# Kernel optimization log

Hardware: AMD Instinct MI355X
Metric: run time of the kernel (lower is better)

The kernel has to match this reference:

```python
import jax, jax.numpy as jnp
import numpy as np

LOG2 = float(np.log(2.0))

def ssp(x):
    # ShiftedSoftplus: softplus(x) - log(2)
    return jax.nn.softplus(x) - LOG2

B, N, F, R, P = 8, 1000, 128, 20, 512000  # batch, atoms, n_atom_basis=n_filters, n_rbf, n_pairs

def setup_inputs() -> dict:
    key = jax.random.key(0)
    ks = jax.random.split(key, 14)
    inv = lambda d: 1.0 / np.sqrt(d)
    return {
        "x": jax.random.normal(ks[0], (B, N, F), dtype=jnp.float32),
        "f_ij": jax.random.normal(ks[1], (P, R), dtype=jnp.float32),
        "idx_i": jax.random.randint(ks[2], (P,), 0, B * N, dtype=jnp.int32),
        "idx_j": jax.random.randint(ks[3], (P,), 0, B * N, dtype=jnp.int32),
        "rcut_ij": jax.random.uniform(ks[4], (P,), dtype=jnp.float32),
        # input_to_feature: Linear(F, F)
        "W_in": jax.random.normal(ks[5], (F, F), dtype=jnp.float32) * inv(F),
        "b_in": jnp.zeros((F,), dtype=jnp.float32),
        # filter_network: Linear(R, F) -> SSP -> Linear(F, F)
        "Wf1": jax.random.normal(ks[6], (R, F), dtype=jnp.float32) * inv(R),
        "bf1": jnp.zeros((F,), dtype=jnp.float32),
        "Wf2": jax.random.normal(ks[7], (F, F), dtype=jnp.float32) * inv(F),
        "bf2": jnp.zeros((F,), dtype=jnp.float32),
        # feature_to_output: Linear(F, F) -> SSP -> Linear(F, F)
        "Wo1": jax.random.normal(ks[8], (F, F), dtype=jnp.float32) * inv(F),
        "bo1": jnp.zeros((F,), dtype=jnp.float32),
        "Wo2": jax.random.normal(ks[9], (F, F), dtype=jnp.float32) * inv(F),
        "bo2": jnp.zeros((F,), dtype=jnp.float32),
    }

def reference(x, f_ij, idx_i, idx_j, rcut_ij,
              W_in, b_in, Wf1, bf1, Wf2, bf2, Wo1, bo1, Wo2, bo2):
    batch, n_atoms = x.shape[0], x.shape[1]
    # input_to_feature
    h = (x @ W_in + b_in).reshape(batch * n_atoms, -1)      # [B*N, F]
    # filter network on radial basis, modulated by cutoff
    Wij = ssp(f_ij @ Wf1 + bf1) @ Wf2 + bf2                 # [P, F]
    Wij = Wij * rcut_ij[:, None]
    # gather neighbor features, elementwise filter, scatter-add to center atom
    x_ij = h[idx_j] * Wij                                   # [P, F]
    agg = jax.ops.segment_sum(x_ij, idx_i, num_segments=batch * n_atoms)  # [B*N, F]
    # feature_to_output
    out = ssp(agg @ Wo1 + bo1) @ Wo2 + bo2
    return out.reshape(batch, n_atoms, 128)
```

## Files before the change

### kernel.cpp

```cpp
#include <hip/hip_runtime.h>
#include <hip/hip_bf16.h>
#include <math.h>

#define FDIM 128
#define RDIM 20
#define BN   8000
#define NPAIR 512000
#define PB   64
#define ROWS 8

typedef __attribute__((ext_vector_type(8))) short short8v;
typedef __attribute__((ext_vector_type(4))) float float4v;

__device__ __forceinline__ float sspf_fast(float x) {
    return fmaxf(x, 0.0f) + __logf(1.0f + __expf(-fabsf(x))) - 0.69314718055994531f;
}
__device__ __forceinline__ float sspf(float x) {
    return fmaxf(x, 0.0f) + log1pf(expf(-fabsf(x))) - 0.69314718055994531f;
}

__device__ __forceinline__ unsigned short bfs(float a) {
    union { __hip_bfloat16 h; unsigned short u; } v;
    v.h = __float2bfloat16(a);
    return v.u;
}
__device__ __forceinline__ unsigned pkbf(float a, float b) {
    union { __hip_bfloat162 h; unsigned u; } v;
    v.h = __float22bfloat162_rn(make_float2(a, b));
    return v.u;
}

__global__ __launch_bounds__(256) void hist_kernel(
    const int* __restrict__ idx_i, int* __restrict__ cnt)
{
    const int p = blockIdx.x * 256 + threadIdx.x;
    if (p < NPAIR) atomicAdd(&cnt[idx_i[p]], 1);
}

__global__ __launch_bounds__(1024) void scan_kernel(
    const int* __restrict__ cnt, int* __restrict__ cursor)
{
    __shared__ int part[1024];
    const int t = threadIdx.x;
    int v[8]; int sum = 0;
    #pragma unroll
    for (int k = 0; k < 8; ++k) {
        const int i = t * 8 + k;
        const int c = (i < BN) ? cnt[i] : 0;
        v[k] = sum; sum += c;
    }
    part[t] = sum;
    __syncthreads();
    for (int off = 1; off < 1024; off <<= 1) {
        const int x = (t >= off) ? part[t - off] : 0;
        __syncthreads();
        part[t] += x;
        __syncthreads();
    }
    const int base = (t == 0) ? 0 : part[t - 1];
    #pragma unroll
    for (int k = 0; k < 8; ++k) {
        const int i = t * 8 + k;
        if (i < BN) cursor[i] = base + v[k];
    }
}

__global__ __launch_bounds__(256) void scatter_kernel(
    const int* __restrict__ idx_i, int* __restrict__ cursor, int* __restrict__ perm)
{
    const int p = blockIdx.x * 256 + threadIdx.x;
    if (p < NPAIR) {
        const int pos = atomicAdd(&cursor[idx_i[p]], 1);
        perm[pos] = p;
    }
}

__global__ __launch_bounds__(256) void scatter_split(
    const int* __restrict__ idx_i, const int* __restrict__ idx_j,
    int* __restrict__ cursor, int4* __restrict__ msorted)
{
    const int p = blockIdx.x * 256 + threadIdx.x;
    if (p < NPAIR) {
        const int ii = idx_i[p];
        const int pos = atomicAdd(&cursor[ii], 1);
        msorted[pos] = make_int4(p, idx_j[p], ii & (ROWS - 1), 0);
    }
}

template<bool SSP, bool BF16OUT>
__global__ __launch_bounds__(256) void rowgemm_kernel(
    const float* __restrict__ A, const float* __restrict__ W,
    const float* __restrict__ bias, void* __restrict__ Cv)
{
    __shared__ float rowlds[16 * 128];
    const int tid = threadIdx.x;
    const int blk = blockIdx.x;
    for (int s = tid; s < 16 * 128; s += 256)
        rowlds[s] = A[blk * 16 * 128 + s];
    __syncthreads();

    const int lane = tid & 63;
    const int wave = tid >> 6;
    const float b0 = bias[lane];
    const float b1 = bias[64 + lane];
    float acc[4][2];
    #pragma unroll
    for (int rr = 0; rr < 4; ++rr) { acc[rr][0] = b0; acc[rr][1] = b1; }

    #pragma unroll 4
    for (int m = 0; m < 128; ++m) {
        const float w0 = W[m * 128 + lane];
        const float w1 = W[m * 128 + 64 + lane];
        #pragma unroll
        for (int rr = 0; rr < 4; ++rr) {
            const float av = rowlds[(wave * 4 + rr) * 128 + m];
            acc[rr][0] = fmaf(av, w0, acc[rr][0]);
            acc[rr][1] = fmaf(av, w1, acc[rr][1]);
        }
    }

    #pragma unroll
    for (int rr = 0; rr < 4; ++rr) {
        const int p = blk * 16 + wave * 4 + rr;
        float v0 = acc[rr][0], v1 = acc[rr][1];
        if (SSP) { v0 = sspf(v0); v1 = sspf(v1); }
        if (BF16OUT) {
            unsigned short* C = (unsigned short*)Cv;
            C[p * 128 + lane]      = bfs(v0);
            C[p * 128 + 64 + lane] = bfs(v1);
        } else {
            float* C = (float*)Cv;
            C[p * 128 + lane]      = v0;
            C[p * 128 + 64 + lane] = v1;
        }
    }
}

__global__ __launch_bounds__(256) void filter_gemm(
    const float* __restrict__ f_ij, const float* __restrict__ rcut,
    const float* __restrict__ Wf1, const float* __restrict__ bf1,
    const float* __restrict__ Wf2, const float* __restrict__ bf2,
    unsigned short* __restrict__ Wij)
{
    __shared__ unsigned short act[64 * 128];
    const int tid = threadIdx.x;
    const int w   = tid >> 6;
    const int l   = tid & 63;
    const int l15 = l & 15;
    const int l4  = l >> 4;
    const int swz = (l15 & 7) << 4;
    const int pbase = blockIdx.x * 64;

    short8v wf1a[2];
    #pragma unroll
    for (int kt2 = 0; kt2 < 2; ++kt2) {
        const int ck = w * 32 + kt2 * 16 + l15;
        #pragma unroll
        for (int e = 0; e < 8; ++e) {
            const int r = l4 * 8 + e;
            const float val = (r < RDIM) ? Wf1[r * 128 + ck] : 0.0f;
            wf1a[kt2][e] = (short)bfs(val);
        }
    }
    short8v wf2a[2][4];
    #pragma unroll
    for (int mt = 0; mt < 2; ++mt) {
        const int c = w * 32 + mt * 16 + l15;
        #pragma unroll
        for (int ks = 0; ks < 4; ++ks) {
            #pragma unroll
            for (int e = 0; e < 8; ++e) {
                const int k = ks * 32 + l4 * 8 + e;
                wf2a[mt][ks][e] = (short)bfs(Wf2[k * 128 + c]);
            }
        }
    }
    float b1v[2][4], b2v[2][4];
    #pragma unroll
    for (int t = 0; t < 2; ++t)
        #pragma unroll
        for (int j = 0; j < 4; ++j) {
            b1v[t][j] = bf1[w * 32 + t * 16 + l4 * 4 + j];
            b2v[t][j] = bf2[w * 32 + t * 16 + l4 * 4 + j];
        }

    float rc[4];
    #pragma unroll
    for (int nt = 0; nt < 4; ++nt)
        rc[nt] = rcut[pbase + nt * 16 + l15];

    short8v ffr[4];
    #pragma unroll
    for (int nt = 0; nt < 4; ++nt) {
        const float* fb = &f_ij[(size_t)(pbase + nt * 16 + l15) * RDIM];
        float4 fa = {0.f, 0.f, 0.f, 0.f}, fc = {0.f, 0.f, 0.f, 0.f};
        if (l4 < 3) fa = *(const float4*)(fb + l4 * 8);
        if (l4 < 2) fc = *(const float4*)(fb + l4 * 8 + 4);
        union { unsigned u[4]; short8v v; } pk;
        pk.u[0] = pkbf(fa.x, fa.y); pk.u[1] = pkbf(fa.z, fa.w);
        pk.u[2] = pkbf(fc.x, fc.y); pk.u[3] = pkbf(fc.z, fc.w);
        ffr[nt] = pk.v;
    }

    #pragma unroll
    for (int kt2 = 0; kt2 < 2; ++kt2) {
        #pragma unroll
        for (int nt = 0; nt < 4; ++nt) {
            float4v acc1 = {0.f, 0.f, 0.f, 0.f};
            acc1 = __builtin_amdgcn_mfma_f32_16x16x32_bf16(wf1a[kt2], ffr[nt], acc1, 0, 0, 0);
            const unsigned lo = pkbf(sspf_fast(acc1[0] + b1v[kt2][0]),
                                     sspf_fast(acc1[1] + b1v[kt2][1]));
            const unsigned hi = pkbf(sspf_fast(acc1[2] + b1v[kt2][2]),
                                     sspf_fast(acc1[3] + b1v[kt2][3]));
            const int row = nt * 16 + l15;
            const int byte = row * 256 + ((w * 64 + kt2 * 32 + l4 * 8) ^ swz);
            *(unsigned long long*)((char*)act + byte) =
                (unsigned long long)lo | ((unsigned long long)hi << 32);
        }
    }
    __syncthreads();

    #pragma unroll
    for (int mt = 0; mt < 2; ++mt) {
        float4v a2[4];
        #pragma unroll
        for (int nt = 0; nt < 4; ++nt) a2[nt] = float4v{0.f, 0.f, 0.f, 0.f};

        #pragma unroll
        for (int ks = 0; ks < 4; ++ks) {
            short8v bfr[4];
            #pragma unroll
            for (int nt = 0; nt < 4; ++nt) {
                const int row = nt * 16 + l15;
                const int byte = row * 256 + ((ks * 64 + l4 * 16) ^ swz);
                bfr[nt] = *(const short8v*)((const char*)act + byte);
            }
            #pragma unroll
            for (int nt = 0; nt < 4; ++nt)
                a2[nt] = __builtin_amdgcn_mfma_f32_16x16x32_bf16(
                    wf2a[mt][ks], bfr[nt], a2[nt], 0, 0, 0);
        }

        #pragma unroll
        for (int nt = 0; nt < 4; ++nt) {
            const size_t p = pbase + nt * 16 + l15;
            uint2 val;
            val.x = pkbf((a2[nt][0] + b2v[mt][0]) * rc[nt],
                         (a2[nt][1] + b2v[mt][1]) * rc[nt]);
            val.y = pkbf((a2[nt][2] + b2v[mt][2]) * rc[nt],
                         (a2[nt][3] + b2v[mt][3]) * rc[nt]);
            *(uint2*)&Wij[p * 128 + w * 32 + mt * 16 + l4 * 4] = val;
        }
    }
}

__global__ __launch_bounds__(256) void pairs_agg(
    const int4* __restrict__ msorted, const unsigned short* __restrict__ Wij,
    const unsigned short* __restrict__ h2, const int* __restrict__ rowEnd,
    float* __restrict__ agg)
{
    __shared__ unsigned short wlds[64 * 128];
    __shared__ unsigned short xbuf[128 * 64];
    __shared__ int           jjs[2][PB];
    __shared__ unsigned char rrs[2][PB];

    const int tid = threadIdx.x;
    const int w   = tid >> 6;
    const int l   = tid & 63;
    const int l15 = l & 15;
    const int l4  = l >> 4;
    const int swz = (l15 & 7) << 4;

    const int row0 = blockIdx.x * ROWS;
    const int s0 = (row0 == 0) ? 0 : rowEnd[row0 - 1];
    const int s1 = rowEnd[row0 + ROWS - 1];

    float4v accD[2];
    accD[0] = float4v{0.f, 0.f, 0.f, 0.f};
    accD[1] = float4v{0.f, 0.f, 0.f, 0.f};

    int tb = 0;
    for (int s = s0; s < s1; s += PB, tb ^= 1) {
        if (tid < PB) {
            const int q  = s + tid;
            const int qc = q < s1 ? q : s1 - 1;
            const int4 m = msorted[qc];
            jjs[tb][tid] = m.y;
            rrs[tb][tid] = (q < s1) ? (unsigned char)m.z : (unsigned char)255;
        }
        {
            const int p4 = tid >> 2, q4 = tid & 3;
            const int q  = s + p4;
            const int qc = q < s1 ? q : s1 - 1;
            const int pid = msorted[qc].x;
            const char* src = (const char*)(Wij + (size_t)pid * 128) + q4 * 64;
            #pragma unroll
            for (int i = 0; i < 4; ++i) {
                const uint4 v = *(const uint4*)(src + i * 16);
                const int byte = p4 * 256 + ((q4 * 64 + i * 16) ^ ((p4 & 7) << 4));
                *(uint4*)((char*)wlds + byte) = v;
            }
        }
        __syncthreads();

        #pragma unroll
        for (int nt = 0; nt < 4; ++nt) {
            const int p   = nt * 16 + l15;
            const int jj  = jjs[tb][p] << 7;
            const int psw = (p & 7) << 4;
            #pragma unroll
            for (int mt = 0; mt < 2; ++mt) {
                const int c0 = w * 32 + mt * 16 + l4 * 4;
                const unsigned long long wv = *(const unsigned long long*)
                    ((const char*)wlds + p * 256 + ((c0 * 2) ^ psw));
                const unsigned long long hv = *(const unsigned long long*)&h2[jj + c0];
                #pragma unroll
                for (int j = 0; j < 4; ++j) {
                    const float wf = __uint_as_float((unsigned)((wv >> (16 * j)) & 0xFFFFULL) << 16);
                    const float hf = __uint_as_float((unsigned)((hv >> (16 * j)) & 0xFFFFULL) << 16);
                    const int c = c0 + j;
                    const int byte = c * 128 + ((p * 2) ^ ((c & 7) << 4));
                    *(unsigned short*)((char*)xbuf + byte) = bfs(hf * wf);
                }
            }
        }
        __syncthreads();

        #pragma unroll
        for (int ks = 0; ks < 2; ++ks) {
            short8v sfr;
            #pragma unroll
            for (int e = 0; e < 8; ++e) {
                const int pr = ks * 32 + l4 * 8 + e;
                sfr[e] = (rrs[tb][pr] == (unsigned char)l15) ? (short)0x3F80 : (short)0;
            }
            #pragma unroll
            for (int mt = 0; mt < 2; ++mt) {
                const int c = w * 32 + mt * 16 + l15;
                const int byte = c * 128 + ((ks * 64 + l4 * 16) ^ swz);
                const short8v xfr = *(const short8v*)((const char*)xbuf + byte);
                accD[mt] = __builtin_amdgcn_mfma_f32_16x16x32_bf16(xfr, sfr, accD[mt], 0, 0, 0);
            }
        }
    }

    if (l15 < ROWS) {
        #pragma unroll
        for (int mt = 0; mt < 2; ++mt) {
            float4 v;
            v.x = accD[mt][0]; v.y = accD[mt][1]; v.z = accD[mt][2]; v.w = accD[mt][3];
            *(float4*)&agg[(size_t)(row0 + l15) * 128 + w * 32 + mt * 16 + l4 * 4] = v;
        }
    }
}

__global__ __launch_bounds__(256) void pairs_mfma_agg(
    const float* __restrict__ f_ij, const int* __restrict__ idx_i,
    const int* __restrict__ idx_j, const float* __restrict__ rcut,
    const float* __restrict__ Wf1, const float* __restrict__ bf1,
    const float* __restrict__ Wf2, const float* __restrict__ bf2,
    const unsigned short* __restrict__ h2, const int* __restrict__ rowEnd,
    const int* __restrict__ perm, float* __restrict__ agg)
{
    __shared__ unsigned short xt[64 * 128];
    __shared__ int   rrs[PB];
    __shared__ int   jjs[PB];
    __shared__ float rcs[PB];

    const int tid = threadIdx.x;
    const int w   = tid >> 6;
    const int l   = tid & 63;
    const int l15 = l & 15;
    const int l4  = l >> 4;
    const int swz = (l15 & 7) << 4;

    const int row0 = blockIdx.x * ROWS;
    const int s0 = (row0 == 0) ? 0 : rowEnd[row0 - 1];
    const int s1 = rowEnd[row0 + ROWS - 1];

    short8v wf1a[2];
    #pragma unroll
    for (int kt2 = 0; kt2 < 2; ++kt2) {
        const int ck = w * 32 + kt2 * 16 + l15;
        #pragma unroll
        for (int e = 0; e < 8; ++e) {
            const int r = l4 * 8 + e;
            const float val = (r < RDIM) ? Wf1[r * 128 + ck] : 0.0f;
            wf1a[kt2][e] = (short)bfs(val);
        }
    }
    short8v wf2a[2][4];
    #pragma unroll
    for (int mt = 0; mt < 2; ++mt) {
        const int c = w * 32 + mt * 16 + l15;
        #pragma unroll
        for (int ks = 0; ks < 4; ++ks) {
            #pragma unroll
            for (int e = 0; e < 8; ++e) {
                const int k = ks * 32 + l4 * 8 + e;
                wf2a[mt][ks][e] = (short)bfs(Wf2[k * 128 + c]);
            }
        }
    }
    float b1v[2][4], b2v[2][4];
    #pragma unroll
    for (int t = 0; t < 2; ++t)
        #pragma unroll
        for (int j = 0; j < 4; ++j) {
            b1v[t][j] = bf1[w * 32 + t * 16 + l4 * 4 + j];
            b2v[t][j] = bf2[w * 32 + t * 16 + l4 * 4 + j];
        }

    float4v accD[2];
    accD[0] = float4v{0.f, 0.f, 0.f, 0.f};
    accD[1] = float4v{0.f, 0.f, 0.f, 0.f};

    for (int s = s0; s < s1; s += PB) {
        __syncthreads();

        if (tid < PB) {
            const int q  = s + tid;
            const int qc = q < s1 ? q : s1 - 1;
            const int pid = perm[qc];
            rrs[tid] = idx_i[pid] - row0;
            jjs[tid] = idx_j[pid];
            rcs[tid] = (q < s1) ? rcut[pid] : 0.0f;
        }

        short8v ffr[4];
        #pragma unroll
        for (int nt = 0; nt < 4; ++nt) {
            const int q = s + nt * 16 + l15;
            const int pid = perm[q < s1 ? q : s1 - 1];
            const float* fb = &f_ij[(size_t)pid * RDIM];
            float4 fa = {0.f, 0.f, 0.f, 0.f}, fc = {0.f, 0.f, 0.f, 0.f};
            if (l4 < 3) fa = *(const float4*)(fb + l4 * 8);
            if (l4 < 2) fc = *(const float4*)(fb + l4 * 8 + 4);
            union { unsigned u[4]; short8v v; } pk;
            pk.u[0] = pkbf(fa.x, fa.y); pk.u[1] = pkbf(fa.z, fa.w);
            pk.u[2] = pkbf(fc.x, fc.y); pk.u[3] = pkbf(fc.z, fc.w);
            ffr[nt] = pk.v;
        }
        __syncthreads();

        unsigned long long hvb[4][2];
        #pragma unroll
        for (int nt = 0; nt < 4; ++nt) {
            const int gj = jjs[nt * 16 + l15] << 7;
            hvb[nt][0] = *(const unsigned long long*)&h2[gj + w * 32 + l4 * 4];
            hvb[nt][1] = *(const unsigned long long*)&h2[gj + w * 32 + 16 + l4 * 4];
        }

        #pragma unroll
        for (int kt2 = 0; kt2 < 2; ++kt2) {
            #pragma unroll
            for (int nt = 0; nt < 4; ++nt) {
                float4v acc1 = {0.f, 0.f, 0.f, 0.f};
                acc1 = __builtin_amdgcn_mfma_f32_16x16x32_bf16(wf1a[kt2], ffr[nt], acc1, 0, 0, 0);
                const unsigned lo = pkbf(sspf_fast(acc1[0] + b1v[kt2][0]),
                                         sspf_fast(acc1[1] + b1v[kt2][1]));
                const unsigned hi = pkbf(sspf_fast(acc1[2] + b1v[kt2][2]),
                                         sspf_fast(acc1[3] + b1v[kt2][3]));
                const int row = nt * 16 + l15;
                const int byte = row * 256 + ((w * 64 + kt2 * 32 + l4 * 8) ^ swz);
                *(unsigned long long*)((char*)xt + byte) =
                    (unsigned long long)lo | ((unsigned long long)hi << 32);
            }
        }
        __syncthreads();

        float4v a2[2][4];
        #pragma unroll
        for (int mt = 0; mt < 2; ++mt)
            #pragma unroll
            for (int nt = 0; nt < 4; ++nt)
                a2[mt][nt] = float4v{0.f, 0.f, 0.f, 0.f};

        #pragma unroll
        for (int ks = 0; ks < 4; ++ks) {
            short8v bfr[4];
            #pragma unroll
            for (int nt = 0; nt < 4; ++nt) {
                const int row = nt * 16 + l15;
                const int byte = row * 256 + ((ks * 64 + l4 * 16) ^ swz);
                bfr[nt] = *(const short8v*)((const char*)xt + byte);
            }
            #pragma unroll
            for (int mt = 0; mt < 2; ++mt)
                #pragma unroll
                for (int nt = 0; nt < 4; ++nt)
                    a2[mt][nt] = __builtin_amdgcn_mfma_f32_16x16x32_bf16(
                        wf2a[mt][ks], bfr[nt], a2[mt][nt], 0, 0, 0);
        }
        __syncthreads();

        #pragma unroll
        for (int nt = 0; nt < 4; ++nt) {
            const int p = nt * 16 + l15;
            const float r = rcs[p];
            #pragma unroll
            for (int mt = 0; mt < 2; ++mt) {
                #pragma unroll
                for (int j = 0; j < 4; ++j) {
                    const int c = w * 32 + mt * 16 + l4 * 4 + j;
                    const float hf = __uint_as_float(
                        (unsigned)((hvb[nt][mt] >> (16 * j)) & 0xFFFFULL) << 16);
                    const float xv = hf * ((a2[mt][nt][j] + b2v[mt][j]) * r);
                    const int byte = c * 128 + ((p * 2) ^ ((c & 7) << 4));
                    *(unsigned short*)((char*)xt + byte) = bfs(xv);
                }
            }
        }
        __syncthreads();

        #pragma unroll
        for (int ks = 0; ks < 2; ++ks) {
            short8v sfr;
            #pragma unroll
            for (int e = 0; e < 8; ++e) {
                const int pr = ks * 32 + l4 * 8 + e;
                sfr[e] = (rrs[pr] == l15) ? (short)0x3F80 : (short)0;
            }
            #pragma unroll
            for (int mt = 0; mt < 2; ++mt) {
                const int c = w * 32 + mt * 16 + l15;
                const int byte = c * 128 + ((ks * 64 + l4 * 16) ^ swz);
                const short8v xfr = *(const short8v*)((const char*)xt + byte);
                accD[mt] = __builtin_amdgcn_mfma_f32_16x16x32_bf16(xfr, sfr, accD[mt], 0, 0, 0);
            }
        }
    }

    if (l15 < ROWS) {
        #pragma unroll
        for (int mt = 0; mt < 2; ++mt) {
            float4 v;
            v.x = accD[mt][0]; v.y = accD[mt][1]; v.z = accD[mt][2]; v.w = accD[mt][3];
            *(float4*)&agg[(size_t)(row0 + l15) * 128 + w * 32 + mt * 16 + l4 * 4] = v;
        }
    }
}

extern "C" void kernel_launch(void* const* d_in, const int* in_sizes, int n_in,
                              void* d_out, int out_size, void* d_ws, size_t ws_size,
                              hipStream_t stream) {
    const float* x     = (const float*)d_in[0];
    const float* f_ij  = (const float*)d_in[1];
    const int*   idx_i = (const int*)  d_in[2];
    const int*   idx_j = (const int*)  d_in[3];
    const float* rcut  = (const float*)d_in[4];
    const float* W_in  = (const float*)d_in[5];
    const float* b_in  = (const float*)d_in[6];
    const float* Wf1   = (const float*)d_in[7];
    const float* bf1   = (const float*)d_in[8];
    const float* Wf2   = (const float*)d_in[9];
    const float* bf2   = (const float*)d_in[10];
    const float* Wo1   = (const float*)d_in[11];
    const float* bo1   = (const float*)d_in[12];
    const float* Wo2   = (const float*)d_in[13];
    const float* bo2   = (const float*)d_in[14];
    float* out = (float*)d_out;

    unsigned short* h2 = (unsigned short*)d_ws;
    float* agg = (float*)((char*)d_ws + 2048000);
    float* t1  = (float*)((char*)d_ws + 2048000 + 4096000);
    int* perm   = (int*)t1;
    int* cnt    = (int*)((char*)t1 + (size_t)NPAIR * 4);
    int* cursor = cnt + 8001;
    int4* msorted      = (int4*)((char*)d_ws + 10240000);
    unsigned short* Wij = (unsigned short*)((char*)d_ws + 10240000 + 8192000);
    const size_t SPLIT_BYTES = 10240000ull + 8192000ull + 131072000ull;

    const bool use_split = (ws_size >= SPLIT_BYTES);

    hipMemsetAsync(cnt, 0, (BN + 1) * sizeof(int), stream);
    hist_kernel<<<NPAIR / 256, 256, 0, stream>>>(idx_i, cnt);
    scan_kernel<<<1, 1024, 0, stream>>>(cnt, cursor);
    if (use_split) {
        scatter_split<<<NPAIR / 256, 256, 0, stream>>>(idx_i, idx_j, cursor, msorted);
    } else {
        scatter_kernel<<<NPAIR / 256, 256, 0, stream>>>(idx_i, cursor, perm);
    }

    rowgemm_kernel<false, true><<<BN / 16, 256, 0, stream>>>(x, W_in, b_in, h2);

    if (use_split) {
        filter_gemm<<<NPAIR / 64, 256, 0, stream>>>(
            f_ij, rcut, Wf1, bf1, Wf2, bf2, Wij);
        pairs_agg<<<BN / ROWS, 256, 0, stream>>>(
            msorted, Wij, h2, cursor, agg);
    } else {
        pairs_mfma_agg<<<BN / ROWS, 256, 0, stream>>>(
            f_ij, idx_i, idx_j, rcut, Wf1, bf1, Wf2, bf2, h2, cursor, perm, agg);
    }

    rowgemm_kernel<true,  false><<<BN / 16, 256, 0, stream>>>(agg, Wo1, bo1, t1);
    rowgemm_kernel<false, false><<<BN / 16, 256, 0, stream>>>(t1, Wo2, bo2, out);
}
```

Baseline: 273.1 us.

## Sort pair data up front, fuse gather-multiply into filter kernel, stream aggregation

The scatter step now writes the radial basis as bf16 in sorted order, plus packed metadata (idx_j, idx_i, rcut). The filter kernel runs on these sorted chunks in a persistent grid and multiplies by the gathered h[idx_j] itself, writing transposed bf16 messages per chunk. Aggregation then just streams those messages with the one-hot MFMA reduction. This removes the random-access Wij gather by pair id and the per-block LDS staging in the aggregation kernel. In exchange it needs a larger workspace and an extra pass that rewrites f_ij in sorted order.

After: 240.3 us. 1.14x faster.

```diff
diff --git a/kernel.cpp b/kernel.cpp
--- a/kernel.cpp
+++ b/kernel.cpp
@@ -8,6 +8,8 @@
 #define NPAIR 512000
 #define PB   64
 #define ROWS 8
+#define NCHUNK (NPAIR / PB)
+#define FILTER_GRID 2048
 
 typedef __attribute__((ext_vector_type(8))) short short8v;
 typedef __attribute__((ext_vector_type(4))) float float4v;
@@ -75,16 +77,30 @@
     }
 }
 
-__global__ __launch_bounds__(256) void scatter_split(
+__global__ __launch_bounds__(256) void scatter_sorted(
     const int* __restrict__ idx_i, const int* __restrict__ idx_j,
-    int* __restrict__ cursor, int4* __restrict__ msorted)
+    const float* __restrict__ rcut, const float* __restrict__ f_ij,
+    int* __restrict__ cursor, int4* __restrict__ meta,
+    unsigned short* __restrict__ fsorted)
 {
     const int p = blockIdx.x * 256 + threadIdx.x;
-    if (p < NPAIR) {
-        const int ii = idx_i[p];
-        const int pos = atomicAdd(&cursor[ii], 1);
-        msorted[pos] = make_int4(p, idx_j[p], ii & (ROWS - 1), 0);
-    }
+    if (p >= NPAIR) return;
+    const int ii = idx_i[p];
+    const int pos = atomicAdd(&cursor[ii], 1);
+    meta[pos] = make_int4(idx_j[p], ii, __float_as_int(rcut[p]), 0);
+
+    const float4* fb = (const float4*)(f_ij + (size_t)p * RDIM);
+    const float4 f0 = fb[0], f1 = fb[1], f2 = fb[2], f3 = fb[3], f4 = fb[4];
+    uint4 d0, d1, d2, d3;
+    d0.x = pkbf(f0.x, f0.y); d0.y = pkbf(f0.z, f0.w);
+    d0.z = pkbf(f1.x, f1.y); d0.w = pkbf(f1.z, f1.w);
+    d1.x = pkbf(f2.x, f2.y); d1.y = pkbf(f2.z, f2.w);
+    d1.z = pkbf(f3.x, f3.y); d1.w = pkbf(f3.z, f3.w);
+    d2.x = pkbf(f4.x, f4.y); d2.y = pkbf(f4.z, f4.w);
+    d2.z = 0; d2.w = 0;
+    d3.x = 0; d3.y = 0; d3.z = 0; d3.w = 0;
+    uint4* dst = (uint4*)(fsorted + (size_t)pos * 32);
+    dst[0] = d0; dst[1] = d1; dst[2] = d2; dst[3] = d3;
 }
 
 template<bool SSP, bool BF16OUT>
@@ -136,20 +152,21 @@
     }
 }
 
-__global__ __launch_bounds__(256) void filter_gemm(
-    const float* __restrict__ f_ij, const float* __restrict__ rcut,
+__global__ __launch_bounds__(256) void filter_sorted(
+    const unsigned short* __restrict__ fsorted, const int4* __restrict__ meta,
+    const unsigned short* __restrict__ h2,
     const float* __restrict__ Wf1, const float* __restrict__ bf1,
     const float* __restrict__ Wf2, const float* __restrict__ bf2,
-    unsigned short* __restrict__ Wij)
+    unsigned short* __restrict__ Xt)
 {
     __shared__ unsigned short act[64 * 128];
+    __shared__ unsigned short xpose[4][32 * 64];
     const int tid = threadIdx.x;
     const int w   = tid >> 6;
     const int l   = tid & 63;
     const int l15 = l & 15;
     const int l4  = l >> 4;
     const int swz = (l15 & 7) << 4;
-    const int pbase = blockIdx.x * 64;
 
     short8v wf1a[2];
     #pragma unroll
@@ -184,47 +201,50 @@
             b2v[t][j] = bf2[w * 32 + t * 16 + l4 * 4 + j];
         }
 
-    float rc[4];
-    #pragma unroll
-    for (int nt = 0; nt < 4; ++nt)
-        rc[nt] = rcut[pbase + nt * 16 + l15];
-
-    short8v ffr[4];
-    #pragma unroll
-    for (int nt = 0; nt < 4; ++nt) {
-        const float* fb = &f_ij[(size_t)(pbase + nt * 16 + l15) * RDIM];
-        float4 fa = {0.f, 0.f, 0.f, 0.f}, fc = {0.f, 0.f, 0.f, 0.f};
-        if (l4 < 3) fa = *(const float4*)(fb + l4 * 8);
-        if (l4 < 2) fc = *(const float4*)(fb + l4 * 8 + 4);
-        union { unsigned u[4]; short8v v; } pk;
-        pk.u[0] = pkbf(fa.x, fa.y); pk.u[1] = pkbf(fa.z, fa.w);
-        pk.u[2] = pkbf(fc.x, fc.y); pk.u[3] = pkbf(fc.z, fc.w);
-        ffr[nt] = pk.v;
-    }
-
-    #pragma unroll
-    for (int kt2 = 0; kt2 < 2; ++kt2) {
+    for (int chunk = blockIdx.x; chunk < NCHUNK; chunk += FILTER_GRID) {
+        const int pbase = chunk * PB;
+
+        short8v ffr[4];
+        float rc[4];
+        int jj[4];
         #pragma unroll
         for (int nt = 0; nt < 4; ++nt) {
-            float4v acc1 = {0.f, 0.f, 0.f, 0.f};
-            acc1 = __builtin_amdgcn_mfma_f32_16x16x32_bf16(wf1a[kt2], ffr[nt], acc1, 0, 0, 0);
-            const unsigned lo = pkbf(sspf_fast(acc1[0] + b1v[kt2][0]),
-                                     sspf_fast(acc1[1] + b1v[kt2][1]));
-            const unsigned hi = pkbf(sspf_fast(acc1[2] + b1v[kt2][2]),
-                                     sspf_fast(acc1[3] + b1v[kt2][3]));
-            const int row = nt * 16 + l15;
-            const int byte = row * 256 + ((w * 64 + kt2 * 32 + l4 * 8) ^ swz);
-            *(unsigned long long*)((char*)act + byte) =
-                (unsigned long long)lo | ((unsigned long long)hi << 32);
-        }
-    }
-    __syncthreads();
-
-    #pragma unroll
-    for (int mt = 0; mt < 2; ++mt) {
-        float4v a2[4];
-        #pragma unroll
-        for (int nt = 0; nt < 4; ++nt) a2[nt] = float4v{0.f, 0.f, 0.f, 0.f};
+            const int q = pbase + nt * 16 + l15;
+            const uint4* fr = (const uint4*)(fsorted + (size_t)q * 32);
+            union { uint4 u; short8v v; } cv;
+            cv.u = fr[l4];
+            ffr[nt] = cv.v;
+            const int4 m = meta[q];
+            jj[nt] = m.x;
+            rc[nt] = __int_as_float(m.z);
+        }
+
+        __syncthreads();
+
+        #pragma unroll
+        for (int kt2 = 0; kt2 < 2; ++kt2) {
+            #pragma unroll
+            for (int nt = 0; nt < 4; ++nt) {
+                float4v acc1 = {0.f, 0.f, 0.f, 0.f};
+                acc1 = __builtin_amdgcn_mfma_f32_16x16x32_bf16(wf1a[kt2], ffr[nt], acc1, 0, 0, 0);
+                const unsigned lo = pkbf(sspf_fast(acc1[0] + b1v[kt2][0]),
+                                         sspf_fast(acc1[1] + b1v[kt2][1]));
+                const unsigned hi = pkbf(sspf_fast(acc1[2] + b1v[kt2][2]),
+                                         sspf_fast(acc1[3] + b1v[kt2][3]));
+                const int row = nt * 16 + l15;
+                const int byte = row * 256 + ((w * 64 + kt2 * 32 + l4 * 8) ^ swz);
+                *(unsigned long long*)((char*)act + byte) =
+                    (unsigned long long)lo | ((unsigned long long)hi << 32);
+            }
+        }
+        __syncthreads();
+
+        float4v a2[2][4];
+        #pragma unroll
+        for (int mt = 0; mt < 2; ++mt)
+            #pragma unroll
+            for (int nt = 0; nt < 4; ++nt)
+                a2[mt][nt] = float4v{0.f, 0.f, 0.f, 0.f};
 
         #pragma unroll
         for (int ks = 0; ks < 4; ++ks) {
@@ -236,109 +256,87 @@
                 bfr[nt] = *(const short8v*)((const char*)act + byte);
             }
             #pragma unroll
-            for (int nt = 0; nt < 4; ++nt)
-                a2[nt] = __builtin_amdgcn_mfma_f32_16x16x32_bf16(
-                    wf2a[mt][ks], bfr[nt], a2[nt], 0, 0, 0);
-        }
-
+            for (int mt = 0; mt < 2; ++mt)
+                #pragma unroll
+                for (int nt = 0; nt < 4; ++nt)
+                    a2[mt][nt] = __builtin_amdgcn_mfma_f32_16x16x32_bf16(
+                        wf2a[mt][ks], bfr[nt], a2[mt][nt], 0, 0, 0);
+        }
+
+        unsigned short* xp = &xpose[w][0];
         #pragma unroll
         for (int nt = 0; nt < 4; ++nt) {
-            const size_t p = pbase + nt * 16 + l15;
-            uint2 val;
-            val.x = pkbf((a2[nt][0] + b2v[mt][0]) * rc[nt],
-                         (a2[nt][1] + b2v[mt][1]) * rc[nt]);
-            val.y = pkbf((a2[nt][2] + b2v[mt][2]) * rc[nt],
-                         (a2[nt][3] + b2v[mt][3]) * rc[nt]);
-            *(uint2*)&Wij[p * 128 + w * 32 + mt * 16 + l4 * 4] = val;
-        }
-    }
-}
-
-__global__ __launch_bounds__(256) void pairs_agg(
-    const int4* __restrict__ msorted, const unsigned short* __restrict__ Wij,
-    const unsigned short* __restrict__ h2, const int* __restrict__ rowEnd,
-    float* __restrict__ agg)
-{
-    __shared__ unsigned short wlds[64 * 128];
-    __shared__ unsigned short xbuf[128 * 64];
-    __shared__ int           jjs[2][PB];
-    __shared__ unsigned char rrs[2][PB];
-
+            const int gj = jj[nt] << 7;
+            const int p  = nt * 16 + l15;
+            #pragma unroll
+            for (int mt = 0; mt < 2; ++mt) {
+                const unsigned long long hv =
+                    *(const unsigned long long*)&h2[gj + w * 32 + mt * 16 + l4 * 4];
+                #pragma unroll
+                for (int j = 0; j < 4; ++j) {
+                    const float hf = __uint_as_float(
+                        (unsigned)((hv >> (16 * j)) & 0xFFFFULL) << 16);
+                    const int cp = mt * 16 + l4 * 4 + j;
+                    const float xv = hf * ((a2[mt][nt][j] + b2v[mt][j]) * rc[nt]);
+                    const int byte = cp * 128 + ((p * 2) ^ ((cp & 7) << 4));
+                    *(unsigned short*)((char*)xp + byte) = bfs(xv);
+                }
+            }
+        }
+
+        char* dst = (char*)Xt + (size_t)chunk * 16384;
+        #pragma unroll
+        for (int i = 0; i < 4; ++i) {
+            const int r  = i * 8 + (l >> 3);
+            const int lb = r * 128 + ((((l & 7) * 16)) ^ ((r & 7) << 4));
+            const uint4 v = *(const uint4*)((const char*)xp + lb);
+            *(uint4*)(dst + (w * 32 + r) * 128 + (l & 7) * 16) = v;
+        }
+    }
+}
+
+__global__ __launch_bounds__(256) void agg_stream(
+    const int4* __restrict__ meta, const unsigned short* __restrict__ Xt,
+    const int* __restrict__ rowEnd, float* __restrict__ agg)
+{
+    __shared__ int rrsF[2][PB];
     const int tid = threadIdx.x;
     const int w   = tid >> 6;
     const int l   = tid & 63;
     const int l15 = l & 15;
     const int l4  = l >> 4;
-    const int swz = (l15 & 7) << 4;
 
     const int row0 = blockIdx.x * ROWS;
     const int s0 = (row0 == 0) ? 0 : rowEnd[row0 - 1];
     const int s1 = rowEnd[row0 + ROWS - 1];
+    const int ch0 = s0 >> 6;
+    const int ch1 = (s1 + PB - 1) >> 6;
 
     float4v accD[2];
     accD[0] = float4v{0.f, 0.f, 0.f, 0.f};
     accD[1] = float4v{0.f, 0.f, 0.f, 0.f};
 
     int tb = 0;
-    for (int s = s0; s < s1; s += PB, tb ^= 1) {
+    for (int ch = ch0; ch < ch1; ++ch, tb ^= 1) {
         if (tid < PB) {
-            const int q  = s + tid;
-            const int qc = q < s1 ? q : s1 - 1;
-            const int4 m = msorted[qc];
-            jjs[tb][tid] = m.y;
-            rrs[tb][tid] = (q < s1) ? (unsigned char)m.z : (unsigned char)255;
-        }
-        {
-            const int p4 = tid >> 2, q4 = tid & 3;
-            const int q  = s + p4;
-            const int qc = q < s1 ? q : s1 - 1;
-            const int pid = msorted[qc].x;
-            const char* src = (const char*)(Wij + (size_t)pid * 128) + q4 * 64;
-            #pragma unroll
-            for (int i = 0; i < 4; ++i) {
-                const uint4 v = *(const uint4*)(src + i * 16);
-                const int byte = p4 * 256 + ((q4 * 64 + i * 16) ^ ((p4 & 7) << 4));
-                *(uint4*)((char*)wlds + byte) = v;
-            }
-        }
-        __syncthreads();
-
-        #pragma unroll
-        for (int nt = 0; nt < 4; ++nt) {
-            const int p   = nt * 16 + l15;
-            const int jj  = jjs[tb][p] << 7;
-            const int psw = (p & 7) << 4;
-            #pragma unroll
-            for (int mt = 0; mt < 2; ++mt) {
-                const int c0 = w * 32 + mt * 16 + l4 * 4;
-                const unsigned long long wv = *(const unsigned long long*)
-                    ((const char*)wlds + p * 256 + ((c0 * 2) ^ psw));
-                const unsigned long long hv = *(const unsigned long long*)&h2[jj + c0];
-                #pragma unroll
-                for (int j = 0; j < 4; ++j) {
-                    const float wf = __uint_as_float((unsigned)((wv >> (16 * j)) & 0xFFFFULL) << 16);
-                    const float hf = __uint_as_float((unsigned)((hv >> (16 * j)) & 0xFFFFULL) << 16);
-                    const int c = c0 + j;
-                    const int byte = c * 128 + ((p * 2) ^ ((c & 7) << 4));
-                    *(unsigned short*)((char*)xbuf + byte) = bfs(hf * wf);
-                }
-            }
-        }
-        __syncthreads();
-
+            const int q = ch * PB + tid;
+            rrsF[tb][tid] = (q < NPAIR) ? (meta[q].y - row0) : -1;
+        }
+        __syncthreads();
+
+        const char* base = (const char*)Xt + (size_t)ch * 16384;
         #pragma unroll
         for (int ks = 0; ks < 2; ++ks) {
             short8v sfr;
             #pragma unroll
             for (int e = 0; e < 8; ++e) {
                 const int pr = ks * 32 + l4 * 8 + e;
-                sfr[e] = (rrs[tb][pr] == (unsigned char)l15) ? (short)0x3F80 : (short)0;
+                sfr[e] = (rrsF[tb][pr] == l15) ? (short)0x3F80 : (short)0;
             }
             #pragma unroll
             for (int mt = 0; mt < 2; ++mt) {
-                const int c = w * 32 + mt * 16 + l15;
-                const int byte = c * 128 + ((ks * 64 + l4 * 16) ^ swz);
-                const short8v xfr = *(const short8v*)((const char*)xbuf + byte);
+                const short8v xfr = *(const short8v*)
+                    (base + (w * 32 + mt * 16 + l15) * 128 + ks * 64 + l4 * 16);
                 accD[mt] = __builtin_amdgcn_mfma_f32_16x16x32_bf16(xfr, sfr, accD[mt], 0, 0, 0);
             }
         }
@@ -563,37 +561,48 @@
 
     unsigned short* h2 = (unsigned short*)d_ws;
     float* agg = (float*)((char*)d_ws + 2048000);
-    float* t1  = (float*)((char*)d_ws + 2048000 + 4096000);
-    int* perm   = (int*)t1;
-    int* cnt    = (int*)((char*)t1 + (size_t)NPAIR * 4);
+    int4* meta = (int4*)((char*)d_ws + 6144000);
+    int* cnt    = (int*)((char*)d_ws + 14336000);
     int* cursor = cnt + 8001;
-    int4* msorted      = (int4*)((char*)d_ws + 10240000);
-    unsigned short* Wij = (unsigned short*)((char*)d_ws + 10240000 + 8192000);
-    const size_t SPLIT_BYTES = 10240000ull + 8192000ull + 131072000ull;
+    unsigned short* fsorted = (unsigned short*)((char*)d_ws + 14400512);
+    unsigned short* Xt      = (unsigned short*)((char*)d_ws + 47168512);
+    float* t1_split = (float*)fsorted;
+    const size_t SPLIT_BYTES = 47168512ull + 131072000ull;
+
+    float* t1_fb = (float*)((char*)d_ws + 6144000);
+    int* perm_fb   = (int*)t1_fb;
+    int* cnt_fb    = (int*)((char*)t1_fb + (size_t)NPAIR * 4);
+    int* cursor_fb = cnt_fb + 8001;
 
     const bool use_split = (ws_size >= SPLIT_BYTES);
 
-    hipMemsetAsync(cnt, 0, (BN + 1) * sizeof(int), stream);
-    hist_kernel<<<NPAIR / 256, 256, 0, stream>>>(idx_i, cnt);
-    scan_kernel<<<1, 1024, 0, stream>>>(cnt, cursor);
     if (use_split) {
-        scatter_split<<<NPAIR / 256, 256, 0, stream>>>(idx_i, idx_j, cursor, msorted);
+        hipMemsetAsync(cnt, 0, (BN + 1) * sizeof(int), stream);
+        hist_kernel<<<NPAIR / 256, 256, 0, stream>>>(idx_i, cnt);
+        scan_kernel<<<1, 1024, 0, stream>>>(cnt, cursor);
+        scatter_sorted<<<NPAIR / 256, 256, 0, stream>>>(
+            idx_i, idx_j, rcut, f_ij, cursor, meta, fsorted);
+
+        rowgemm_kernel<false, true><<<BN / 16, 256, 0, stream>>>(x, W_in, b_in, h2);
+
+        filter_sorted<<<FILTER_GRID, 256, 0, stream>>>(
+            fsorted, meta, h2, Wf1, bf1, Wf2, bf2, Xt);
+        agg_stream<<<BN / ROWS, 256, 0, stream>>>(meta, Xt, cursor, agg);
+
+        rowgemm_kernel<true,  false><<<BN / 16, 256, 0, stream>>>(agg, Wo1, bo1, t1_split);
+        rowgemm_kernel<false, false><<<BN / 16, 256, 0, stream>>>(t1_split, Wo2, bo2, out);
     } else {
-        scatter_kernel<<<NPAIR / 256, 256, 0, stream>>>(idx_i, cursor, perm);
-    }
-
-    rowgemm_kernel<false, true><<<BN / 16, 256, 0, stream>>>(x, W_in, b_in, h2);
-
-    if (use_split) {
-        filter_gemm<<<NPAIR / 64, 256, 0, stream>>>(
-            f_ij, rcut, Wf1, bf1, Wf2, bf2, Wij);
-        pairs_agg<<<BN / ROWS, 256, 0, stream>>>(
-            msorted, Wij, h2, cursor, agg);
-    } else {
+        hipMemsetAsync(cnt_fb, 0, (BN + 1) * sizeof(int), stream);
+        hist_kernel<<<NPAIR / 256, 256, 0, stream>>>(idx_i, cnt_fb);
+        scan_kernel<<<1, 1024, 0, stream>>>(cnt_fb, cursor_fb);
+        scatter_kernel<<<NPAIR / 256, 256, 0, stream>>>(idx_i, cursor_fb, perm_fb);
+
+        rowgemm_kernel<false, true><<<BN / 16, 256, 0, stream>>>(x, W_in, b_in, h2);
+
         pairs_mfma_agg<<<BN / ROWS, 256, 0, stream>>>(
-            f_ij, idx_i, idx_j, rcut, Wf1, bf1, Wf2, bf2, h2, cursor, perm, agg);
-    }
-
-    rowgemm_kernel<true,  false><<<BN / 16, 256, 0, stream>>>(agg, Wo1, bo1, t1);
-    rowgemm_kernel<false, false><<<BN / 16, 256, 0, stream>>>(t1, Wo2, bo2, out);
-}
+            f_ij, idx_i, idx_j, rcut, Wf1, bf1, Wf2, bf2, h2, cursor_fb, perm_fb, agg);
+
+        rowgemm_kernel<true,  false><<<BN / 16, 256, 0, stream>>>(agg, Wo1, bo1, t1_fb);
+        rowgemm_kernel<false, false><<<BN / 16, 256, 0, stream>>>(t1_fb, Wo2, bo2, out);
+    }
+}
```
